# Kernel optimization log

Measured on AMD Instinct MI355X. Metric: run time of the kernel, lower is better.

Reference implementation:

```python
import jax, jax.numpy as jnp
import numpy as np

TOTAL_BITS = 8  # current_bits at init; < 16 so quantization is active


def _quantize_static(w, bits, f):
    # f is a static Python int (grid-search candidate)
    int_bits = bits - f - 1
    step = 2.0 ** (-f)
    q_min = -(2.0 ** int_bits)
    q_max = 2.0 ** int_bits - step
    return jnp.round(jnp.clip(w, q_min, q_max) / step) * step


def setup_inputs() -> dict:
    key = jax.random.key(0)
    x = jax.random.normal(key, (8, 4096, 4096), dtype=jnp.float32)
    return {"x": x}


def reference(x):
    b = TOTAL_BITS
    xd = jax.lax.stop_gradient(x)
    # grid search over fractional bits f in [0, b-1]: per-candidate quantization MSE
    mses = jnp.stack([jnp.mean((xd - _quantize_static(xd, b, f)) ** 2) for f in range(b)])
    best_f = jnp.argmin(mses)
    # quantize with the (traced) best f
    fi = best_f.astype(x.dtype)
    step = jnp.exp2(-fi)
    int_bits = jnp.asarray(b, x.dtype) - fi - 1.0
    q_min = -jnp.exp2(int_bits)
    q_max = jnp.exp2(int_bits) - step
    x_q = jnp.round(jnp.clip(x, q_min, q_max) / step) * step
    # STE: forward uses quantized values, backward is identity
    return x + jax.lax.stop_gradient(x_q - x)
```

## Files before the change

kernel.cpp:

```cpp
#include <hip/hip_runtime.h>

#define TOTAL_BITS 8
#define MSE_BLOCKS 2048


__global__ __launch_bounds__(256) void fpq_mse(const float* __restrict__ x,
                                               float* __restrict__ ws,
                                               long long n) {
    float acc[TOTAL_BITS];
#pragma unroll
    for (int f = 0; f < TOTAL_BITS; ++f) acc[f] = 0.0f;

    const long long nvec = n >> 2;
    const float4* __restrict__ xv = (const float4*)x;
    const long long tid = (long long)blockIdx.x * blockDim.x + threadIdx.x;
    const long long stride = (long long)gridDim.x * blockDim.x;

    for (long long i = tid; i < nvec; i += stride) {
        float4 v = xv[i];
        float vals[4] = {v.x, v.y, v.z, v.w};
#pragma unroll
        for (int j = 0; j < 4; ++j) {
            float w = vals[j];
#pragma unroll
            for (int f = 0; f < TOTAL_BITS; ++f) {
                const float scale = (float)(1 << f);
                const float step  = 1.0f / (float)(1 << f);
                const float base  = (float)(1 << (TOTAL_BITS - 1 - f));
                const float qmin  = -base;
                const float qmax  = base - step;
                float c = fminf(fmaxf(w, qmin), qmax);
                float r = rintf(c * scale);
                float e = fmaf(-r, step, w);
                acc[f] = fmaf(e, e, acc[f]);
            }
        }
    }
    for (long long i = (nvec << 2) + tid; i < n; i += stride) {
        float w = x[i];
#pragma unroll
        for (int f = 0; f < TOTAL_BITS; ++f) {
            const float scale = (float)(1 << f);
            const float step  = 1.0f / (float)(1 << f);
            const float base  = (float)(1 << (TOTAL_BITS - 1 - f));
            const float qmin  = -base;
            const float qmax  = base - step;
            float c = fminf(fmaxf(w, qmin), qmax);
            float r = rintf(c * scale);
            float e = fmaf(-r, step, w);
            acc[f] = fmaf(e, e, acc[f]);
        }
    }

    __shared__ float s[TOTAL_BITS];
    if (threadIdx.x < TOTAL_BITS) s[threadIdx.x] = 0.0f;
    __syncthreads();
#pragma unroll
    for (int f = 0; f < TOTAL_BITS; ++f) {
        float v = acc[f];
#pragma unroll
        for (int off = 32; off > 0; off >>= 1) v += __shfl_down(v, off, 64);
        if ((threadIdx.x & 63) == 0) atomicAdd(&s[f], v);
    }
    __syncthreads();
    if (threadIdx.x < TOTAL_BITS)
        ws[16 + 8 * (long long)blockIdx.x + threadIdx.x] = s[threadIdx.x];
}

__global__ void fpq_select(float* __restrict__ ws, int nblocks) {
    __shared__ float s[TOTAL_BITS];
    if (threadIdx.x < TOTAL_BITS) s[threadIdx.x] = 0.0f;
    __syncthreads();
    const int f = threadIdx.x & 7;
    float acc = 0.0f;
    for (int b = threadIdx.x >> 3; b < nblocks; b += (int)blockDim.x >> 3)
        acc += ws[16 + 8 * (long long)b + f];
    atomicAdd(&s[f], acc);
    __syncthreads();
    if (threadIdx.x == 0) {
        int best = 0;
        float bm = s[0];
        for (int g = 1; g < TOTAL_BITS; ++g) {
            if (s[g] < bm) { bm = s[g]; best = g; }
        }
        float scale = (float)(1 << best);
        float step  = 1.0f / scale;
        float base  = (float)(1 << (TOTAL_BITS - 1 - best));
        ws[8]  = step;
        ws[9]  = scale;
        ws[10] = -base;
        ws[11] = base - step;
    }
}

__global__ __launch_bounds__(256) void fpq_quant(const float* __restrict__ x,
                                                 float* __restrict__ out,
                                                 const float* __restrict__ ws,
                                                 long long n) {
    const float step  = ws[8];
    const float scale = ws[9];
    const float qmin  = ws[10];
    const float qmax  = ws[11];

    const long long nvec = n >> 2;
    const float4* __restrict__ xv = (const float4*)x;
    float4* __restrict__ ov = (float4*)out;
    const long long tid = (long long)blockIdx.x * blockDim.x + threadIdx.x;
    const long long stride = (long long)gridDim.x * blockDim.x;

    for (long long i = tid; i < nvec; i += stride) {
        float4 v = xv[i];
        float4 o;
        o.x = rintf(fminf(fmaxf(v.x, qmin), qmax) * scale) * step;
        o.y = rintf(fminf(fmaxf(v.y, qmin), qmax) * scale) * step;
        o.z = rintf(fminf(fmaxf(v.z, qmin), qmax) * scale) * step;
        o.w = rintf(fminf(fmaxf(v.w, qmin), qmax) * scale) * step;
        ov[i] = o;
    }
    for (long long i = (nvec << 2) + tid; i < n; i += stride) {
        out[i] = rintf(fminf(fmaxf(x[i], qmin), qmax) * scale) * step;
    }
}

extern "C" void kernel_launch(void* const* d_in, const int* in_sizes, int n_in,
                              void* d_out, int out_size, void* d_ws, size_t ws_size,
                              hipStream_t stream) {
    const float* x = (const float*)d_in[0];
    float* out = (float*)d_out;
    float* ws = (float*)d_ws;
    const long long n = (long long)in_sizes[0];

    fpq_mse<<<MSE_BLOCKS, 256, 0, stream>>>(x, ws, n);
    fpq_select<<<1, 256, 0, stream>>>(ws, MSE_BLOCKS);
    fpq_quant<<<8192, 256, 0, stream>>>(x, out, ws, n);
}
```

Before: 1.007 ms.

## Clamp in scaled domain, widen per-thread chunks, reverse quant order for L2 reuse

```diff
diff --git a/kernel.cpp b/kernel.cpp
--- a/kernel.cpp
+++ b/kernel.cpp
@@ -2,86 +2,89 @@
 
 #define TOTAL_BITS 8
 #define MSE_BLOCKS 2048
+#define QUANT_BLOCKS 2048
 
+
+typedef float f32x4 __attribute__((ext_vector_type(4)));
 
 __global__ __launch_bounds__(256) void fpq_mse(const float* __restrict__ x,
                                                float* __restrict__ ws,
                                                long long n) {
+    constexpr float QLO = -(float)(1 << (TOTAL_BITS - 1));
+    constexpr float QHI = (float)(1 << (TOTAL_BITS - 1)) - 1.0f;
+
     float acc[TOTAL_BITS];
 #pragma unroll
     for (int f = 0; f < TOTAL_BITS; ++f) acc[f] = 0.0f;
 
-    const long long nvec = n >> 2;
+    const long long nch = n >> 3;
     const float4* __restrict__ xv = (const float4*)x;
     const long long tid = (long long)blockIdx.x * blockDim.x + threadIdx.x;
     const long long stride = (long long)gridDim.x * blockDim.x;
 
-    for (long long i = tid; i < nvec; i += stride) {
-        float4 v = xv[i];
-        float vals[4] = {v.x, v.y, v.z, v.w};
+    for (long long i = tid; i < nch; i += stride) {
+        const float4 a = xv[2 * i];
+        const float4 b = xv[2 * i + 1];
+        const float vals[8] = {a.x, a.y, a.z, a.w, b.x, b.y, b.z, b.w};
 #pragma unroll
-        for (int j = 0; j < 4; ++j) {
-            float w = vals[j];
+        for (int j = 0; j < 8; ++j) {
+            const float w = vals[j];
 #pragma unroll
             for (int f = 0; f < TOTAL_BITS; ++f) {
                 const float scale = (float)(1 << f);
                 const float step  = 1.0f / (float)(1 << f);
-                const float base  = (float)(1 << (TOTAL_BITS - 1 - f));
-                const float qmin  = -base;
-                const float qmax  = base - step;
-                float c = fminf(fmaxf(w, qmin), qmax);
-                float r = rintf(c * scale);
+                float s = w * scale;
+                float c = fminf(fmaxf(s, QLO), QHI);
+                float r = rintf(c);
                 float e = fmaf(-r, step, w);
                 acc[f] = fmaf(e, e, acc[f]);
             }
         }
     }
-    for (long long i = (nvec << 2) + tid; i < n; i += stride) {
-        float w = x[i];
+    for (long long i = (nch << 3) + tid; i < n; i += stride) {
+        const float w = x[i];
 #pragma unroll
         for (int f = 0; f < TOTAL_BITS; ++f) {
             const float scale = (float)(1 << f);
             const float step  = 1.0f / (float)(1 << f);
-            const float base  = (float)(1 << (TOTAL_BITS - 1 - f));
-            const float qmin  = -base;
-            const float qmax  = base - step;
-            float c = fminf(fmaxf(w, qmin), qmax);
-            float r = rintf(c * scale);
+            float s = w * scale;
+            float c = fminf(fmaxf(s, QLO), QHI);
+            float r = rintf(c);
             float e = fmaf(-r, step, w);
             acc[f] = fmaf(e, e, acc[f]);
         }
     }
 
-    __shared__ float s[TOTAL_BITS];
-    if (threadIdx.x < TOTAL_BITS) s[threadIdx.x] = 0.0f;
+    __shared__ float sm[TOTAL_BITS];
+    if (threadIdx.x < TOTAL_BITS) sm[threadIdx.x] = 0.0f;
     __syncthreads();
 #pragma unroll
     for (int f = 0; f < TOTAL_BITS; ++f) {
         float v = acc[f];
 #pragma unroll
         for (int off = 32; off > 0; off >>= 1) v += __shfl_down(v, off, 64);
-        if ((threadIdx.x & 63) == 0) atomicAdd(&s[f], v);
+        if ((threadIdx.x & 63) == 0) atomicAdd(&sm[f], v);
     }
     __syncthreads();
     if (threadIdx.x < TOTAL_BITS)
-        ws[16 + 8 * (long long)blockIdx.x + threadIdx.x] = s[threadIdx.x];
+        ws[16 + 8 * (long long)blockIdx.x + threadIdx.x] = sm[threadIdx.x];
 }
 
 __global__ void fpq_select(float* __restrict__ ws, int nblocks) {
-    __shared__ float s[TOTAL_BITS];
-    if (threadIdx.x < TOTAL_BITS) s[threadIdx.x] = 0.0f;
+    __shared__ float sm[TOTAL_BITS];
+    if (threadIdx.x < TOTAL_BITS) sm[threadIdx.x] = 0.0f;
     __syncthreads();
     const int f = threadIdx.x & 7;
     float acc = 0.0f;
     for (int b = threadIdx.x >> 3; b < nblocks; b += (int)blockDim.x >> 3)
         acc += ws[16 + 8 * (long long)b + f];
-    atomicAdd(&s[f], acc);
+    atomicAdd(&sm[f], acc);
     __syncthreads();
     if (threadIdx.x == 0) {
         int best = 0;
-        float bm = s[0];
+        float bm = sm[0];
         for (int g = 1; g < TOTAL_BITS; ++g) {
-            if (s[g] < bm) { bm = s[g]; best = g; }
+            if (sm[g] < bm) { bm = sm[g]; best = g; }
         }
         float scale = (float)(1 << best);
         float step  = 1.0f / scale;
@@ -97,28 +100,35 @@
                                                  float* __restrict__ out,
                                                  const float* __restrict__ ws,
                                                  long long n) {
+    constexpr float QLO = -(float)(1 << (TOTAL_BITS - 1));
+    constexpr float QHI = (float)(1 << (TOTAL_BITS - 1)) - 1.0f;
     const float step  = ws[8];
     const float scale = ws[9];
-    const float qmin  = ws[10];
-    const float qmax  = ws[11];
 
-    const long long nvec = n >> 2;
+    const long long nch = n >> 3;
     const float4* __restrict__ xv = (const float4*)x;
-    float4* __restrict__ ov = (float4*)out;
+    f32x4* __restrict__ ov = (f32x4*)out;
     const long long tid = (long long)blockIdx.x * blockDim.x + threadIdx.x;
     const long long stride = (long long)gridDim.x * blockDim.x;
 
-    for (long long i = tid; i < nvec; i += stride) {
-        float4 v = xv[i];
-        float4 o;
-        o.x = rintf(fminf(fmaxf(v.x, qmin), qmax) * scale) * step;
-        o.y = rintf(fminf(fmaxf(v.y, qmin), qmax) * scale) * step;
-        o.z = rintf(fminf(fmaxf(v.z, qmin), qmax) * scale) * step;
-        o.w = rintf(fminf(fmaxf(v.w, qmin), qmax) * scale) * step;
-        ov[i] = o;
+    for (long long k = tid; k < nch; k += stride) {
+        const long long i = nch - 1 - k;
+        const float4 a = xv[2 * i];
+        const float4 b = xv[2 * i + 1];
+        f32x4 oa, ob;
+        oa.x = rintf(fminf(fmaxf(a.x * scale, QLO), QHI)) * step;
+        oa.y = rintf(fminf(fmaxf(a.y * scale, QLO), QHI)) * step;
+        oa.z = rintf(fminf(fmaxf(a.z * scale, QLO), QHI)) * step;
+        oa.w = rintf(fminf(fmaxf(a.w * scale, QLO), QHI)) * step;
+        ob.x = rintf(fminf(fmaxf(b.x * scale, QLO), QHI)) * step;
+        ob.y = rintf(fminf(fmaxf(b.y * scale, QLO), QHI)) * step;
+        ob.z = rintf(fminf(fmaxf(b.z * scale, QLO), QHI)) * step;
+        ob.w = rintf(fminf(fmaxf(b.w * scale, QLO), QHI)) * step;
+        __builtin_nontemporal_store(oa, &ov[2 * i]);
+        __builtin_nontemporal_store(ob, &ov[2 * i + 1]);
     }
-    for (long long i = (nvec << 2) + tid; i < n; i += stride) {
-        out[i] = rintf(fminf(fmaxf(x[i], qmin), qmax) * scale) * step;
+    for (long long i = (nch << 3) + tid; i < n; i += stride) {
+        out[i] = rintf(fminf(fmaxf(x[i] * scale, QLO), QHI)) * step;
     }
 }
 
@@ -132,5 +142,5 @@
 
     fpq_mse<<<MSE_BLOCKS, 256, 0, stream>>>(x, ws, n);
     fpq_select<<<1, 256, 0, stream>>>(ws, MSE_BLOCKS);
-    fpq_quant<<<8192, 256, 0, stream>>>(x, out, ws, n);
+    fpq_quant<<<QUANT_BLOCKS, 256, 0, stream>>>(x, out, ws, n);
 }
```

Result: slower. 1.032 ms (+2.5%).
